# Kernel tuning notes

Measured on AMD Instinct MI355X. Metric: run time of the kernel, lower is better.

## Reference

```python
import jax, jax.numpy as jnp
import numpy as np

N = 80000        # nodes
E = 1280000      # edges (avg degree 16)
D_IN, H1, H2, D_OUT = 64, 64, 64, 64


def _glorot(key, fan_in, fan_out):
    s = np.sqrt(6.0 / (fan_in + fan_out)).astype(np.float32)
    return jax.random.uniform(key, (fan_in, fan_out), jnp.float32, -s, s)


def setup_inputs() -> dict:
    key = jax.random.key(0)
    ks = jax.random.split(key, 5)
    X = jax.random.normal(ks[0], (N, D_IN), jnp.float32)
    edge_index = jax.random.randint(ks[1], (2, E), 0, N, dtype=jnp.int32).astype(jnp.int64)
    W1 = _glorot(ks[2], D_IN, H1)
    W2 = _glorot(ks[3], H1, H2)
    W3 = _glorot(ks[4], H2, D_OUT)
    b1 = jnp.zeros((H1,), jnp.float32)
    b2 = jnp.zeros((H2,), jnp.float32)
    b3 = jnp.zeros((D_OUT,), jnp.float32)
    return {"X": X, "edge_index": edge_index,
            "W1": W1, "b1": b1, "W2": W2, "b2": b2, "W3": W3, "b3": b3}


def _gcn_conv(x, W, b, src, dst, n):
    """PyG GCNConv: symmetric-normalized mean over A + I, then linear + bias.
    x' = D^{-1/2} (A + I) D^{-1/2} (x W) + b, deg counts self-loops."""
    x = x @ W                                   # [N, F_out]
    # in-degree including self loop (edge weights are 1)
    deg = jnp.ones((n,), x.dtype).at[dst].add(1.0)
    dinv = jax.lax.rsqrt(deg)                   # deg >= 1 always
    coef = dinv[src] * dinv[dst]                # [E]
    msg = x[src] * coef[:, None]                # [E, F_out] gather
    agg = jnp.zeros_like(x).at[dst].add(msg)    # scatter-add to targets
    agg = agg + x * (dinv * dinv)[:, None]      # self-loop contribution
    return agg + b


def reference(X, edge_index, W1, b1, W2, b2, W3, b3):
    src, dst = edge_index[0], edge_index[1]
    n = X.shape[0]
    h = jax.nn.relu(_gcn_conv(X, W1, b1, src, dst, n))
    h = jax.nn.relu(_gcn_conv(h, W2, b2, src, dst, n))
    out = _gcn_conv(h, W3, b3, src, dst, n)     # no activation on last layer
    return out
```

## Files before the change

kernel.cpp:

```cpp
#include <hip/hip_runtime.h>
#include <hip/hip_fp16.h>

#define NN 80000
#define NE 1280000
#define F  64
#define BSH 9
#define NB  157
#define CAP 12288
#define EPB 5120
#define EPT 20
#define PBLK (NE / EPB)
#define LBLK (NN / 64)

typedef _Float16 half_t;
typedef _Float16 half8 __attribute__((ext_vector_type(8)));
typedef float f32x4 __attribute__((ext_vector_type(4)));
typedef unsigned int uint_t;

__global__ void detect_idx64(const int* __restrict__ idx, int* __restrict__ flag) {
    __shared__ int allzero;
    if (threadIdx.x == 0) allzero = 1;
    __syncthreads();
    if (idx[2 * threadIdx.x + 1] != 0) allzero = 0;
    __syncthreads();
    if (threadIdx.x == 0) *flag = allzero;
}

__device__ __forceinline__ int ld_src(const int* __restrict__ idx, int e, int is64) {
    return is64 ? idx[2 * e] : idx[e];
}
__device__ __forceinline__ int ld_dst(const int* __restrict__ idx, int e, int is64) {
    return is64 ? idx[2 * NE + 2 * e] : idx[NE + e];
}

__global__ __launch_bounds__(256) void partition_kernel(
        const int* __restrict__ idx, const int* __restrict__ flag,
        int* __restrict__ bcur, int* __restrict__ ebuf) {
    __shared__ int cnt[NB];
    __shared__ int lbase[NB];
    __shared__ int gbase[NB];
    __shared__ int lds_val[EPB];
    __shared__ int lds_gaddr[EPB];
    int tid = threadIdx.x;
    for (int i = tid; i < NB; i += 256) cnt[i] = 0;
    __syncthreads();
    int is64 = *flag;
    int e0 = blockIdx.x * EPB;
    int val[EPT], br[EPT];
    #pragma unroll
    for (int j = 0; j < EPT; ++j) {
        int e = e0 + j * 256 + tid;
        int s = ld_src(idx, e, is64);
        int d = ld_dst(idx, e, is64);
        int b = d >> BSH;
        val[j] = ((d & ((1 << BSH) - 1)) << 17) | s;
        int r = atomicAdd(&cnt[b], 1);
        br[j] = (b << 13) | r;
    }
    __syncthreads();
    if (tid < 64) {
        int carry = 0;
        for (int base = 0; base < NB; base += 64) {
            int i2 = base + tid;
            int v = (i2 < NB) ? cnt[i2] : 0;
            int incl = v;
            #pragma unroll
            for (int d2 = 1; d2 < 64; d2 <<= 1) {
                int t = __shfl_up(incl, d2, 64);
                if (tid >= d2) incl += t;
            }
            if (i2 < NB) lbase[i2] = carry + incl - v;
            carry += __shfl(incl, 63);
        }
    } else if (tid - 64 < NB) {
        int b = tid - 64;
        gbase[b] = atomicAdd(&bcur[b], cnt[b]);
    }
    __syncthreads();
    #pragma unroll
    for (int j = 0; j < EPT; ++j) {
        int b = br[j] >> 13, r = br[j] & 8191;
        int slot = lbase[b] + r;
        int g = gbase[b] + r;
        lds_val[slot]   = val[j];
        lds_gaddr[slot] = (g < CAP) ? (b * CAP + g) : -1;
    }
    __syncthreads();
    for (int i = tid; i < EPB; i += 256) {
        int a = lds_gaddr[i];
        if (a >= 0) ebuf[a] = lds_val[i];
    }
}

__global__ __launch_bounds__(256) void bucket_sort_kernel(
        const int* __restrict__ bcur, const int* __restrict__ ebuf,
        int* __restrict__ edata, int* __restrict__ row_ptr,
        float* __restrict__ dinv) {
    __shared__ int cnt[512];
    __shared__ int off[512];
    __shared__ int lds_out[CAP];
    __shared__ int ebase_s;
    int b = blockIdx.x, tid = threadIdx.x;
    cnt[tid] = 0; cnt[tid + 256] = 0;
    if (tid < 64) {
        int carry = 0;
        for (int base = 0; base < NB; base += 64) {
            int i2 = base + tid;
            int v = (i2 < NB) ? min(bcur[i2], CAP) : 0;
            int incl = v;
            #pragma unroll
            for (int d2 = 1; d2 < 64; d2 <<= 1) {
                int t = __shfl_up(incl, d2, 64);
                if (tid >= d2) incl += t;
            }
            if (i2 == b) ebase_s = carry + incl - v;
            carry += __shfl(incl, 63);
        }
    }
    __syncthreads();
    int bcnt = min(bcur[b], CAP);
    int ebase = ebase_s;
    const int* src = ebuf + b * CAP;
    for (int i = tid; i < bcnt; i += 256)
        atomicAdd(&cnt[src[i] >> 17], 1);
    __syncthreads();
    if (tid < 64) {
        int carry = 0;
        #pragma unroll
        for (int base = 0; base < 512; base += 64) {
            int v = cnt[base + tid];
            int incl = v;
            #pragma unroll
            for (int d2 = 1; d2 < 64; d2 <<= 1) {
                int t = __shfl_up(incl, d2, 64);
                if (tid >= d2) incl += t;
            }
            off[base + tid] = carry + incl - v;
            carry += __shfl(incl, 63);
        }
    }
    __syncthreads();
    int n0 = b << BSH;
    for (int i = tid; i < 512; i += 256) {
        int n = n0 + i;
        if (n < NN) {
            row_ptr[n] = ebase + off[i];
            dinv[n] = rsqrtf((float)cnt[i] + 1.f);
        } else if (n == NN) {
            row_ptr[NN] = ebase + off[i];
        }
    }
    __syncthreads();
    for (int i = tid; i < bcnt; i += 256) {
        int w = src[i];
        int pos = atomicAdd(&off[w >> 17], 1);
        lds_out[pos] = w & 0x1FFFF;
    }
    __syncthreads();
    for (int i = tid; i < bcnt; i += 256)
        edata[ebase + i] = lds_out[i];
}

__global__ void prescale_kernel(const float* __restrict__ x, const float* __restrict__ dinv,
                                half_t* __restrict__ y) {
    int tid = blockIdx.x * blockDim.x + threadIdx.x;
    if (tid >= NN * 16) return;
    int n = tid >> 4, q = tid & 15;
    float c = dinv[n];
    float4 v = ((const float4*)(x + (size_t)n * F))[q];
    half_t h[4] = { (half_t)(v.x * c), (half_t)(v.y * c),
                    (half_t)(v.z * c), (half_t)(v.w * c) };
    ((uint2*)(y + (size_t)n * F))[q] = *(uint2*)h;
}

__device__ __forceinline__ float2 h2f2(uint_t u) {
    __half2 h = *(__half2*)&u;
    return __half22float2(h);
}

template <int RELU, int SCALE, int LAST>
__global__ __launch_bounds__(256) void gcn_layer(
        const half_t* __restrict__ y, const int* __restrict__ edata,
        const int* __restrict__ row_ptr, const float* __restrict__ dinv,
        const float* __restrict__ W, const float* __restrict__ bias,
        half_t* __restrict__ out_h, float* __restrict__ out_f32) {
    __shared__ half_t Wt[64][72];
    __shared__ half_t xt[64][72];
    int tid = threadIdx.x;
    for (int i = tid; i < 4096; i += 256) {
        int k = i >> 6, n2 = i & 63;
        Wt[n2][k] = (half_t)W[i];
    }
    int wv = tid >> 6, lane = tid & 63;
    int sub = lane >> 4, fl = lane & 15;
    int n0 = blockIdx.x * 64;
    for (int i = 0; i < 16; ++i) {
        int n = n0 + wv * 16 + i;
        int p0 = row_ptr[n], p1 = row_ptr[n + 1];
        float a0 = 0.f, a1 = 0.f, a2 = 0.f, a3 = 0.f;
        for (int base = p0; base < p1; base += 16) {
            int s[4]; float m[4];
            #pragma unroll
            for (int j = 0; j < 4; ++j) {
                int q = base + j * 4 + sub;
                int qc = q < p1 ? q : p1 - 1;
                s[j] = edata[qc];
                m[j] = (q < p1) ? 1.f : 0.f;
            }
            uint2 u[4];
            #pragma unroll
            for (int j = 0; j < 4; ++j)
                u[j] = ((const uint2*)(y + (size_t)s[j] * F))[fl];
            #pragma unroll
            for (int j = 0; j < 4; ++j) {
                float2 lo = h2f2(u[j].x), hi = h2f2(u[j].y);
                a0 = fmaf(m[j], lo.x, a0);
                a1 = fmaf(m[j], lo.y, a1);
                a2 = fmaf(m[j], hi.x, a2);
                a3 = fmaf(m[j], hi.y, a3);
            }
        }
        a0 += __shfl_down(a0, 32); a1 += __shfl_down(a1, 32);
        a2 += __shfl_down(a2, 32); a3 += __shfl_down(a3, 32);
        a0 += __shfl_down(a0, 16); a1 += __shfl_down(a1, 16);
        a2 += __shfl_down(a2, 16); a3 += __shfl_down(a3, 16);
        if (sub == 0) {
            float dv = dinv[n];
            uint2 us = ((const uint2*)(y + (size_t)n * F))[fl];
            float2 slo = h2f2(us.x), shi = h2f2(us.y);
            half_t h[4] = { (half_t)(dv * (a0 + slo.x)), (half_t)(dv * (a1 + slo.y)),
                            (half_t)(dv * (a2 + shi.x)), (half_t)(dv * (a3 + shi.y)) };
            ((uint2*)&xt[wv * 16 + i][0])[fl] = *(uint2*)h;
        }
    }
    __syncthreads();
    int m = lane & 15, q = lane >> 4;
    const half_t* arow = &xt[wv * 16 + m][q * 8];
    half8 A0 = *(const half8*)arow;
    half8 A1 = *(const half8*)(arow + 32);
    #pragma unroll
    for (int ct = 0; ct < 4; ++ct) {
        const half_t* brow = &Wt[ct * 16 + m][q * 8];
        half8 B0 = *(const half8*)brow;
        half8 B1 = *(const half8*)(brow + 32);
        f32x4 c = {0.f, 0.f, 0.f, 0.f};
        c = __builtin_amdgcn_mfma_f32_16x16x32_f16(A0, B0, c, 0, 0, 0);
        c = __builtin_amdgcn_mfma_f32_16x16x32_f16(A1, B1, c, 0, 0, 0);
        float bv = bias[ct * 16 + m];
        #pragma unroll
        for (int r = 0; r < 4; ++r) {
            int row = n0 + wv * 16 + q * 4 + r;
            float v = c[r] + bv;
            if (RELU) v = fmaxf(v, 0.f);
            if (SCALE) v *= dinv[row];
            int col = ct * 16 + m;
            if (LAST) out_f32[(size_t)row * F + col] = v;
            else      out_h[(size_t)row * F + col] = (half_t)v;
        }
    }
}

extern "C" void kernel_launch(void* const* d_in, const int* in_sizes, int n_in,
                              void* d_out, int out_size, void* d_ws, size_t ws_size,
                              hipStream_t stream) {
    const float* X  = (const float*)d_in[0];
    const int*  idx = (const int*)d_in[1];
    const float* W1 = (const float*)d_in[2];
    const float* b1 = (const float*)d_in[3];
    const float* W2 = (const float*)d_in[4];
    const float* b2 = (const float*)d_in[5];
    const float* W3 = (const float*)d_in[6];
    const float* b3 = (const float*)d_in[7];
    float* out = (float*)d_out;

    char* ws = (char*)d_ws;
    int*    flag    = (int*)(ws + 0);
    int*    bcur    = (int*)(ws + 256);
    int*    row_ptr = (int*)(ws + 1024);
    float*  dinv    = (float*)(ws + 321280);
    int*    edata   = (int*)(ws + 641536);
    half_t* ybufA   = (half_t*)(ws + 5761536);
    half_t* ybufB   = (half_t*)(ws + 16001536);
    int*    ebuf    = (int*)(ws + 26241536);

    hipMemsetAsync(bcur, 0, NB * sizeof(int), stream);
    detect_idx64<<<1, 1024, 0, stream>>>(idx, flag);
    partition_kernel<<<PBLK, 256, 0, stream>>>(idx, flag, bcur, ebuf);
    bucket_sort_kernel<<<NB, 256, 0, stream>>>(bcur, ebuf, edata, row_ptr, dinv);
    prescale_kernel<<<(NN * 16) / 256, 256, 0, stream>>>(X, dinv, ybufA);

    gcn_layer<1, 1, 0><<<LBLK, 256, 0, stream>>>(
        ybufA, edata, row_ptr, dinv, W1, b1, ybufB, nullptr);
    gcn_layer<1, 1, 0><<<LBLK, 256, 0, stream>>>(
        ybufB, edata, row_ptr, dinv, W2, b2, ybufA, nullptr);
    gcn_layer<0, 0, 1><<<LBLK, 256, 0, stream>>>(
        ybufA, edata, row_ptr, dinv, W3, b3, nullptr, out);
}
```

Measured before the change: 246.5 us.

## Split fused gather+GEMM layer into separate gather and MFMA GEMM kernels

Splits each fused GCN layer into two kernels. The first is a gather kernel with one node per wavefront and a deeper unroll of 8 edge loads per lane group. The second is a standalone MFMA GEMM kernel over 128-row tiles. This targets the serial per-wave loop over 16 nodes and raises the number of independent gathers in flight, at the cost of an extra fp16 round trip of the aggregated features through global memory. It also folds the bucket-counter memset into the detect kernel to drop one launch.

```diff
diff --git a/kernel.cpp b/kernel.cpp
--- a/kernel.cpp
+++ b/kernel.cpp
@@ -10,18 +10,24 @@
 #define EPB 5120
 #define EPT 20
 #define PBLK (NE / EPB)
-#define LBLK (NN / 64)
 
 typedef _Float16 half_t;
 typedef _Float16 half8 __attribute__((ext_vector_type(8)));
 typedef float f32x4 __attribute__((ext_vector_type(4)));
 typedef unsigned int uint_t;
 
-__global__ void detect_idx64(const int* __restrict__ idx, int* __restrict__ flag) {
+__device__ __forceinline__ float2 h2f2(uint_t u) {
+    __half2 h = *(__half2*)&u;
+    return __half22float2(h);
+}
+
+__global__ void detect_idx64(const int* __restrict__ idx, int* __restrict__ flag,
+                             int* __restrict__ bcur) {
     __shared__ int allzero;
     if (threadIdx.x == 0) allzero = 1;
     __syncthreads();
     if (idx[2 * threadIdx.x + 1] != 0) allzero = 0;
+    if (threadIdx.x < NB) bcur[threadIdx.x] = 0;
     __syncthreads();
     if (threadIdx.x == 0) *flag = allzero;
 }
@@ -173,89 +179,95 @@
     ((uint2*)(y + (size_t)n * F))[q] = *(uint2*)h;
 }
 
-__device__ __forceinline__ float2 h2f2(uint_t u) {
-    __half2 h = *(__half2*)&u;
-    return __half22float2(h);
+__global__ __launch_bounds__(256) void gather_kernel(const half_t* __restrict__ y,
+        const int* __restrict__ edata, const int* __restrict__ row_ptr,
+        const float* __restrict__ dinv, half_t* __restrict__ agg) {
+    int n = blockIdx.x * 4 + (threadIdx.x >> 6);
+    int lane = threadIdx.x & 63;
+    int sub = lane >> 4, fl = lane & 15;
+    int p0 = row_ptr[n], p1 = row_ptr[n + 1];
+    float a0 = 0.f, a1 = 0.f, a2 = 0.f, a3 = 0.f;
+    for (int base = p0; base < p1; base += 32) {
+        int s[8]; float m[8];
+        #pragma unroll
+        for (int j = 0; j < 8; ++j) {
+            int q = base + j * 4 + sub;
+            int qc = q < p1 ? q : p1 - 1;
+            s[j] = edata[qc];
+            m[j] = (q < p1) ? 1.f : 0.f;
+        }
+        uint2 u[8];
+        #pragma unroll
+        for (int j = 0; j < 8; ++j)
+            u[j] = ((const uint2*)(y + (size_t)s[j] * F))[fl];
+        #pragma unroll
+        for (int j = 0; j < 8; ++j) {
+            float2 lo = h2f2(u[j].x), hi = h2f2(u[j].y);
+            a0 = fmaf(m[j], lo.x, a0);
+            a1 = fmaf(m[j], lo.y, a1);
+            a2 = fmaf(m[j], hi.x, a2);
+            a3 = fmaf(m[j], hi.y, a3);
+        }
+    }
+    a0 += __shfl_down(a0, 32); a1 += __shfl_down(a1, 32);
+    a2 += __shfl_down(a2, 32); a3 += __shfl_down(a3, 32);
+    a0 += __shfl_down(a0, 16); a1 += __shfl_down(a1, 16);
+    a2 += __shfl_down(a2, 16); a3 += __shfl_down(a3, 16);
+    if (sub == 0) {
+        float dv = dinv[n];
+        uint2 us = ((const uint2*)(y + (size_t)n * F))[fl];
+        float2 slo = h2f2(us.x), shi = h2f2(us.y);
+        half_t h[4] = { (half_t)(dv * (a0 + slo.x)), (half_t)(dv * (a1 + slo.y)),
+                        (half_t)(dv * (a2 + shi.x)), (half_t)(dv * (a3 + shi.y)) };
+        ((uint2*)(agg + (size_t)n * F))[fl] = *(uint2*)h;
+    }
 }
 
 template <int RELU, int SCALE, int LAST>
-__global__ __launch_bounds__(256) void gcn_layer(
-        const half_t* __restrict__ y, const int* __restrict__ edata,
-        const int* __restrict__ row_ptr, const float* __restrict__ dinv,
-        const float* __restrict__ W, const float* __restrict__ bias,
+__global__ __launch_bounds__(256) void gemm_mfma(
+        const half_t* __restrict__ A, const float* __restrict__ W,
+        const float* __restrict__ bias, const float* __restrict__ dinv,
         half_t* __restrict__ out_h, float* __restrict__ out_f32) {
     __shared__ half_t Wt[64][72];
-    __shared__ half_t xt[64][72];
+    __shared__ half_t xt[128][72];
     int tid = threadIdx.x;
     for (int i = tid; i < 4096; i += 256) {
         int k = i >> 6, n2 = i & 63;
         Wt[n2][k] = (half_t)W[i];
     }
+    int n0 = blockIdx.x * 128;
+    for (int i2 = tid; i2 < 2048; i2 += 256) {
+        int r = i2 >> 4, c = i2 & 15;
+        ((uint2*)&xt[r][0])[c] = ((const uint2*)(A + (size_t)(n0 + r) * F))[c];
+    }
+    __syncthreads();
     int wv = tid >> 6, lane = tid & 63;
-    int sub = lane >> 4, fl = lane & 15;
-    int n0 = blockIdx.x * 64;
-    for (int i = 0; i < 16; ++i) {
-        int n = n0 + wv * 16 + i;
-        int p0 = row_ptr[n], p1 = row_ptr[n + 1];
-        float a0 = 0.f, a1 = 0.f, a2 = 0.f, a3 = 0.f;
-        for (int base = p0; base < p1; base += 16) {
-            int s[4]; float m[4];
+    int m = lane & 15, q = lane >> 4;
+    #pragma unroll
+    for (int rt = 0; rt < 2; ++rt) {
+        int rbase = wv * 32 + rt * 16;
+        const half_t* arow = &xt[rbase + m][q * 8];
+        half8 A0 = *(const half8*)arow;
+        half8 A1 = *(const half8*)(arow + 32);
+        #pragma unroll
+        for (int ct = 0; ct < 4; ++ct) {
+            const half_t* brow = &Wt[ct * 16 + m][q * 8];
+            half8 B0 = *(const half8*)brow;
+            half8 B1 = *(const half8*)(brow + 32);
+            f32x4 c = {0.f, 0.f, 0.f, 0.f};
+            c = __builtin_amdgcn_mfma_f32_16x16x32_f16(A0, B0, c, 0, 0, 0);
+            c = __builtin_amdgcn_mfma_f32_16x16x32_f16(A1, B1, c, 0, 0, 0);
+            float bv = bias[ct * 16 + m];
             #pragma unroll
-            for (int j = 0; j < 4; ++j) {
-                int q = base + j * 4 + sub;
-                int qc = q < p1 ? q : p1 - 1;
-                s[j] = edata[qc];
-                m[j] = (q < p1) ? 1.f : 0.f;
+            for (int r = 0; r < 4; ++r) {
+                int row = n0 + rbase + q * 4 + r;
+                float v = c[r] + bv;
+                if (RELU) v = fmaxf(v, 0.f);
+                if (SCALE) v *= dinv[row];
+                int col = ct * 16 + m;
+                if (LAST) out_f32[(size_t)row * F + col] = v;
+                else      out_h[(size_t)row * F + col] = (half_t)v;
             }
-            uint2 u[4];
-            #pragma unroll
-            for (int j = 0; j < 4; ++j)
-                u[j] = ((const uint2*)(y + (size_t)s[j] * F))[fl];
-            #pragma unroll
-            for (int j = 0; j < 4; ++j) {
-                float2 lo = h2f2(u[j].x), hi = h2f2(u[j].y);
-                a0 = fmaf(m[j], lo.x, a0);
-                a1 = fmaf(m[j], lo.y, a1);
-                a2 = fmaf(m[j], hi.x, a2);
-                a3 = fmaf(m[j], hi.y, a3);
-            }
-        }
-        a0 += __shfl_down(a0, 32); a1 += __shfl_down(a1, 32);
-        a2 += __shfl_down(a2, 32); a3 += __shfl_down(a3, 32);
-        a0 += __shfl_down(a0, 16); a1 += __shfl_down(a1, 16);
-        a2 += __shfl_down(a2, 16); a3 += __shfl_down(a3, 16);
-        if (sub == 0) {
-            float dv = dinv[n];
-            uint2 us = ((const uint2*)(y + (size_t)n * F))[fl];
-            float2 slo = h2f2(us.x), shi = h2f2(us.y);
-            half_t h[4] = { (half_t)(dv * (a0 + slo.x)), (half_t)(dv * (a1 + slo.y)),
-                            (half_t)(dv * (a2 + shi.x)), (half_t)(dv * (a3 + shi.y)) };
-            ((uint2*)&xt[wv * 16 + i][0])[fl] = *(uint2*)h;
-        }
-    }
-    __syncthreads();
-    int m = lane & 15, q = lane >> 4;
-    const half_t* arow = &xt[wv * 16 + m][q * 8];
-    half8 A0 = *(const half8*)arow;
-    half8 A1 = *(const half8*)(arow + 32);
-    #pragma unroll
-    for (int ct = 0; ct < 4; ++ct) {
-        const half_t* brow = &Wt[ct * 16 + m][q * 8];
-        half8 B0 = *(const half8*)brow;
-        half8 B1 = *(const half8*)(brow + 32);
-        f32x4 c = {0.f, 0.f, 0.f, 0.f};
-        c = __builtin_amdgcn_mfma_f32_16x16x32_f16(A0, B0, c, 0, 0, 0);
-        c = __builtin_amdgcn_mfma_f32_16x16x32_f16(A1, B1, c, 0, 0, 0);
-        float bv = bias[ct * 16 + m];
-        #pragma unroll
-        for (int r = 0; r < 4; ++r) {
-            int row = n0 + wv * 16 + q * 4 + r;
-            float v = c[r] + bv;
-            if (RELU) v = fmaxf(v, 0.f);
-            if (SCALE) v *= dinv[row];
-            int col = ct * 16 + m;
-            if (LAST) out_f32[(size_t)row * F + col] = v;
-            else      out_h[(size_t)row * F + col] = (half_t)v;
         }
     }
 }
@@ -283,16 +295,18 @@
     half_t* ybufB   = (half_t*)(ws + 16001536);
     int*    ebuf    = (int*)(ws + 26241536);
 
-    hipMemsetAsync(bcur, 0, NB * sizeof(int), stream);
-    detect_idx64<<<1, 1024, 0, stream>>>(idx, flag);
+    detect_idx64<<<1, 1024, 0, stream>>>(idx, flag, bcur);
     partition_kernel<<<PBLK, 256, 0, stream>>>(idx, flag, bcur, ebuf);
     bucket_sort_kernel<<<NB, 256, 0, stream>>>(bcur, ebuf, edata, row_ptr, dinv);
     prescale_kernel<<<(NN * 16) / 256, 256, 0, stream>>>(X, dinv, ybufA);
 
-    gcn_layer<1, 1, 0><<<LBLK, 256, 0, stream>>>(
-        ybufA, edata, row_ptr, dinv, W1, b1, ybufB, nullptr);
-    gcn_layer<1, 1, 0><<<LBLK, 256, 0, stream>>>(
-        ybufB, edata, row_ptr, dinv, W2, b2, ybufA, nullptr);
-    gcn_layer<0, 0, 1><<<LBLK, 256, 0, stream>>>(
-        ybufA, edata, row_ptr, dinv, W3, b3, nullptr, out);
-}
+    const int gBlocks = NN / 4;
+    const int mBlocks = NN / 128;
+
+    gather_kernel<<<gBlocks, 256, 0, stream>>>(ybufA, edata, row_ptr, dinv, ybufB);
+    gemm_mfma<1, 1, 0><<<mBlocks, 256, 0, stream>>>(ybufB, W1, b1, dinv, ybufA, nullptr);
+    gather_kernel<<<gBlocks, 256, 0, stream>>>(ybufA, edata, row_ptr, dinv, ybufB);
+    gemm_mfma<1, 1, 0><<<mBlocks, 256, 0, stream>>>(ybufB, W2, b2, dinv, ybufA, nullptr);
+    gather_kernel<<<gBlocks, 256, 0, stream>>>(ybufA, edata, row_ptr, dinv, ybufB);
+    gemm_mfma<0, 0, 1><<<mBlocks, 256, 0, stream>>>(ybufB, W3, b3, dinv, nullptr, out);
+}
```

Result: no change. 250.6 us (+1.7%).
